# Optimization experiments

Hardware: AMD Instinct MI355X
Metric: run time of the kernel (lower is better)

Reference implementation:

```python
import jax, jax.numpy as jnp
import numpy as np

N_NODES = 20000
IN_DIM = 256
HID = 128
N_CLASSES = 64
N_EDGES = 320000
EPS_BN = 1e-5


def setup_inputs() -> dict:
    key = jax.random.key(0)
    ks = jax.random.split(key, 24)
    s = 0.1
    inp = {}
    inp['x'] = jax.random.normal(ks[0], (N_NODES, IN_DIM), dtype=jnp.float32)
    inp['edge_index'] = jax.random.randint(ks[1], (2, N_EDGES), 0, N_NODES, dtype=jnp.int32)
    # GATConv 1: in=IN_DIM, out=HID per head, heads=4, concat=False
    inp['W1'] = s * jax.random.normal(ks[2], (IN_DIM, 4 * HID), dtype=jnp.float32)
    inp['a_src1'] = s * jax.random.normal(ks[3], (4, HID), dtype=jnp.float32)
    inp['a_dst1'] = s * jax.random.normal(ks[4], (4, HID), dtype=jnp.float32)
    inp['b1'] = jnp.zeros((HID,), jnp.float32)
    # GATConv 2: in=HID, out=HID per head, heads=4, concat=False
    inp['W2'] = s * jax.random.normal(ks[5], (HID, 4 * HID), dtype=jnp.float32)
    inp['a_src2'] = s * jax.random.normal(ks[6], (4, HID), dtype=jnp.float32)
    inp['a_dst2'] = s * jax.random.normal(ks[7], (4, HID), dtype=jnp.float32)
    inp['b2'] = jnp.zeros((HID,), jnp.float32)
    # GATConv 3: heads=1, concat=True (default)
    inp['W3'] = s * jax.random.normal(ks[8], (HID, HID), dtype=jnp.float32)
    inp['a_src3'] = s * jax.random.normal(ks[9], (1, HID), dtype=jnp.float32)
    inp['a_dst3'] = s * jax.random.normal(ks[10], (1, HID), dtype=jnp.float32)
    inp['b3'] = jnp.zeros((HID,), jnp.float32)
    # BatchNorm (eval-mode running stats)
    for i, k in zip((1, 2), (ks[11], ks[12])):
        inp[f'bn{i}_g'] = jnp.ones((HID,), jnp.float32)
        inp[f'bn{i}_b'] = jnp.zeros((HID,), jnp.float32)
        inp[f'bn{i}_m'] = 0.01 * jax.random.normal(k, (HID,), dtype=jnp.float32)
        inp[f'bn{i}_v'] = jnp.ones((HID,), jnp.float32)
    # classifier MLP
    inp['l1_w'] = s * jax.random.normal(ks[13], (HID, HID), dtype=jnp.float32)
    inp['l1_b'] = jnp.zeros((HID,), jnp.float32)
    inp['l2_w'] = s * jax.random.normal(ks[14], (HID, HID // 2), dtype=jnp.float32)
    inp['l2_b'] = jnp.zeros((HID // 2,), jnp.float32)
    inp['l3_w'] = s * jax.random.normal(ks[15], (HID // 2, N_CLASSES), dtype=jnp.float32)
    inp['l3_b'] = jnp.zeros((N_CLASSES,), jnp.float32)
    return inp


def _gat(x, src, dst, W, a_src, a_dst, b, heads, out_ch, concat):
    """PyG GATConv (with self-loops already appended to src/dst)."""
    n = x.shape[0]
    h = (x @ W).reshape(n, heads, out_ch)            # [N,H,C]
    alpha_s = jnp.sum(h * a_src[None], axis=-1)       # [N,H]
    alpha_d = jnp.sum(h * a_dst[None], axis=-1)       # [N,H]
    e = jax.nn.leaky_relu(alpha_s[src] + alpha_d[dst], 0.2)  # [E,H]
    # segment softmax over incoming edges of each destination node
    m = jax.ops.segment_max(e, dst, num_segments=n)
    m = jnp.where(jnp.isfinite(m), m, 0.0)
    ex = jnp.exp(e - m[dst])
    den = jax.ops.segment_sum(ex, dst, num_segments=n)
    alpha = ex / (den[dst] + 1e-16)                   # [E,H]
    msg = h[src] * alpha[:, :, None]                  # [E,H,C]
    out = jax.ops.segment_sum(msg, dst, num_segments=n)  # [N,H,C]
    out = out.reshape(n, heads * out_ch) if concat else out.mean(axis=1)
    return out + b


def _bn_eval(x, g, b, m, v):
    return g * (x - m) * jax.lax.rsqrt(v + EPS_BN) + b


def reference(x, edge_index, W1, a_src1, a_dst1, b1, W2, a_src2, a_dst2, b2,
              W3, a_src3, a_dst3, b3, bn1_g, bn1_b, bn1_m, bn1_v,
              bn2_g, bn2_b, bn2_m, bn2_v, l1_w, l1_b, l2_w, l2_b, l3_w, l3_b):
    n = x.shape[0]
    loops = jnp.arange(n, dtype=edge_index.dtype)
    src = jnp.concatenate([edge_index[0], loops])
    dst = jnp.concatenate([edge_index[1], loops])

    h = _gat(x, src, dst, W1, a_src1, a_dst1, b1, 4, HID, False)
    h = jax.nn.relu(_bn_eval(h, bn1_g, bn1_b, bn1_m, bn1_v))
    h = _gat(h, src, dst, W2, a_src2, a_dst2, b2, 4, HID, False)
    h = jax.nn.relu(_bn_eval(h, bn2_g, bn2_b, bn2_m, bn2_v))
    h = _gat(h, src, dst, W3, a_src3, a_dst3, b3, 1, HID, True)

    h = jax.nn.relu(h @ l1_w + l1_b)
    h = jax.nn.relu(h @ l2_w + l2_b)
    return jax.nn.sigmoid(h @ l3_w + l3_b)  # [N, num_labels]
```

## Files before the change

### kernel.cpp

```cpp
#include <hip/hip_runtime.h>
#include <cstdint>
#include <cstddef>

#define NN 20000
#define CAP 96

typedef __bf16 bf16_t;
typedef __bf16 bf16x8 __attribute__((ext_vector_type(8)));
typedef float f32x4 __attribute__((ext_vector_type(4)));

#define AS1 __attribute__((address_space(1)))
#define AS3 __attribute__((address_space(3)))

__device__ __forceinline__ float lrelu(float x) { return x >= 0.f ? x : 0.2f * x; }
__device__ __forceinline__ float bflo(uint32_t u) { return __uint_as_float(u << 16); }
__device__ __forceinline__ float bfhi(uint32_t u) { return __uint_as_float(u & 0xffff0000u); }

__device__ __forceinline__ uint32_t pack2bf(float a, float b) {
  bf16_t x = (bf16_t)a, y = (bf16_t)b;
  uint16_t ux = __builtin_bit_cast(uint16_t, x);
  uint16_t uy = __builtin_bit_cast(uint16_t, y);
  return (uint32_t)ux | ((uint32_t)uy << 16);
}


struct WDesc { const float* W; bf16_t* Bt; int K; int Cw; int H; float scale; int b0; };
struct WPack { WDesc d[4]; };

struct Prep1Args {
  WPack wp;
  const float *W1, *as1, *ad1, *W2, *as2, *ad2, *W3, *as3, *ad3;
  float *P1, *P2, *P3;
  const float *W3m, *L1w, *b3v, *l1b;
  bf16_t* M3t; float* bm;
  const int* ei; int E, N, EB;
  int* cnt; int* col;
};

__global__ __launch_bounds__(256) void prep1(Prep1Args a) {
  __shared__ float tile[32][33];
  const int b = blockIdx.x;
  const int t = threadIdx.x;

  if (b < 204) {
    int i = 3;
#pragma unroll
    for (int k = 2; k >= 0; --k)
      if (b < a.wp.d[k + 1].b0) i = k;
    const WDesc de = a.wp.d[i];
    const int bi = b - de.b0;
    const int ktiles = de.K / 32;
    const int kt = bi % ktiles, rt = bi / ktiles;
    const int gc = rt * 32;
    const int h = gc / de.Cw, c0 = gc % de.Cw;
    const int tx = t & 31, ty = t >> 5;
#pragma unroll
    for (int r = 0; r < 32; r += 8)
      tile[ty + r][tx] = de.W[(size_t)(kt * 32 + ty + r) * (de.H * de.Cw) + h * de.Cw + c0 + tx];
    __syncthreads();
#pragma unroll
    for (int r = 0; r < 32; r += 8)
      de.Bt[(size_t)(c0 + ty + r) * (de.H * de.K) + h * de.K + kt * 32 + tx] =
          (bf16_t)(de.scale * tile[tx][ty + r]);
  } else if (b < 716) {
    const int kk = b - 204;
    const float *W, *asrc, *adst;
    float* P;
    int K, H, k;
    if (kk < 256)      { W = a.W1; asrc = a.as1; adst = a.ad1; P = a.P1; K = 256; H = 4; k = kk; }
    else if (kk < 384) { W = a.W2; asrc = a.as2; adst = a.ad2; P = a.P2; K = 128; H = 4; k = kk - 256; }
    else               { W = a.W3; asrc = a.as3; adst = a.ad3; P = a.P3; K = 128; H = 1; k = kk - 384; }
    for (int j = 0; j < 2 * H; ++j) {
      const int h = (j < H) ? j : j - H;
      const float* av = (j < H) ? asrc : adst;
      float pv = 0.f;
      if (t < 128) pv = W[(size_t)k * (H * 128) + h * 128 + t] * av[h * 128 + t];
#pragma unroll
      for (int d = 1; d < 64; d <<= 1) pv += __shfl_xor(pv, d);
      if (t == 0 || t == 64) tile[0][t >> 6] = pv;
      __syncthreads();
      if (t == 0) P[j * K + k] = tile[0][0] + tile[0][1];
      __syncthreads();
    }
  } else if (b < 780) {
    const int idx = (b - 716) * 256 + t;
    const int k = idx >> 7, c = idx & 127;
    float s = 0.f;
    for (int m = 0; m < 128; ++m) s += a.W3m[k * 128 + m] * a.L1w[m * 128 + c];
    a.M3t[c * 128 + k] = (bf16_t)s;
    if (k == 0) {
      float tt = a.l1b[c];
      for (int m = 0; m < 128; ++m) tt += a.b3v[m] * a.L1w[m * 128 + c];
      a.bm[c] = tt;
    }
  } else {
    const int i = (b - 780) * 256 + t;
    if (i < a.E + a.N) {
      int src, dst;
      if (i < a.E) { src = a.ei[i]; dst = a.ei[a.E + i]; }
      else         { src = i - a.E; dst = src; }
      int slot = atomicAdd(&a.cnt[dst], 1);
      a.col[(size_t)dst * CAP + slot] = src;
    }
  }
}


__global__ __launch_bounds__(256) void cast_alpha(const float* __restrict__ x,
                                                  const float* __restrict__ P1,
                                                  bf16_t* __restrict__ xb,
                                                  float* __restrict__ asadA) {
  const int b = blockIdx.x, t = threadIdx.x;
  const int wv = t >> 6, lane = t & 63;
  const int n = b * 4 + wv;
  const float4 v = *(const float4*)&x[(size_t)n * 256 + lane * 4];
  uint2 ov;
  ov.x = pack2bf(v.x, v.y);
  ov.y = pack2bf(v.z, v.w);
  *(uint2*)&xb[(size_t)n * 256 + lane * 4] = ov;
  float s[8];
#pragma unroll
  for (int j = 0; j < 8; ++j) {
    const float4 pj = *(const float4*)&P1[j * 256 + lane * 4];
    s[j] = v.x * pj.x + v.y * pj.y + v.z * pj.z + v.w * pj.w;
  }
#pragma unroll
  for (int j = 0; j < 8; ++j)
#pragma unroll
    for (int d = 1; d < 64; d <<= 1) s[j] += __shfl_xor(s[j], d);
  if (lane == 0) {
#pragma unroll
    for (int j = 0; j < 8; ++j) asadA[(size_t)n * 8 + j] = s[j];
  }
}


template <int ACT, int J, typename OUT_T>
__global__ __launch_bounds__(256) void gemm_mfma(const bf16_t* __restrict__ A,
                                                 const bf16_t* __restrict__ Bt,
                                                 const float* __restrict__ bias,
                                                 const float* __restrict__ bng,
                                                 const float* __restrict__ bnb,
                                                 const float* __restrict__ bnm,
                                                 const float* __restrict__ bnv,
                                                 OUT_T* __restrict__ C,
                                                 const float* __restrict__ Pa,
                                                 float* __restrict__ asad,
                                                 int M, int N, int K) {
  constexpr int TM = 32, TN = 128, BK = 64;
  constexpr int NRA = (TM * BK * 2) / 4096;
  constexpr int NRB = (TN * BK * 2) / 4096;
  __shared__ __align__(16) bf16_t As[TM * BK];
  __shared__ __align__(16) bf16_t Bs[TN * BK];

  const int t = threadIdx.x;
  const int wave = t >> 6, lane = t & 63;
  const int ln15 = lane & 15, quad = lane >> 4;
  const int bm = blockIdx.x * TM;
  const int wm = (wave >> 1) * 16;
  const int wn = (wave & 1) * 64;
  const int rowLimA = M - 1 - bm;
  const size_t strideAB = (size_t)K * 2;

  f32x4 acc[4];
#pragma unroll
  for (int ni = 0; ni < 4; ++ni) acc[ni] = (f32x4){0.f, 0.f, 0.f, 0.f};

  const char* gA = (const char*)(A + (size_t)bm * K);
  const char* gB = (const char*)Bt;

  for (int k0 = 0; k0 < K; k0 += BK) {
#pragma unroll
    for (int r = 0; r < NRA; ++r) {
      int base = (wave * NRA + r) * 1024;
      int flat = base + lane * 16;
      int row = flat >> 7;
      int grow = row < rowLimA ? row : rowLimA;
      const char* gp = gA + (size_t)grow * strideAB + (size_t)(k0 * 2) + (flat & 127);
      __builtin_amdgcn_global_load_lds((const AS1 void*)gp,
                                       (AS3 void*)((char*)As + base), 16, 0, 0);
    }
#pragma unroll
    for (int r = 0; r < NRB; ++r) {
      int base = (wave * NRB + r) * 1024;
      int flat = base + lane * 16;
      int row = flat >> 7;
      const char* gp = gB + (size_t)row * strideAB + (size_t)(k0 * 2) + (flat & 127);
      __builtin_amdgcn_global_load_lds((const AS1 void*)gp,
                                       (AS3 void*)((char*)Bs + base), 16, 0, 0);
    }
    __syncthreads();
#pragma unroll
    for (int kk = 0; kk < BK; kk += 32) {
      bf16x8 af, bfr[4];
      af = *(const bf16x8*)&As[(wm + ln15) * BK + kk + quad * 8];
#pragma unroll
      for (int ni = 0; ni < 4; ++ni)
        bfr[ni] = *(const bf16x8*)&Bs[(wn + ni * 16 + ln15) * BK + kk + quad * 8];
#pragma unroll
      for (int ni = 0; ni < 4; ++ni)
        acc[ni] = __builtin_amdgcn_mfma_f32_16x16x32_bf16(af, bfr[ni], acc[ni], 0, 0, 0);
    }
    __syncthreads();
  }

  {
    int r0 = bm + wm + quad * 4;
#pragma unroll
    for (int ni = 0; ni < 4; ++ni) {
      int c = wn + ni * 16 + ln15;
      float bv = bias ? bias[c] : 0.f;
      float sc = 1.f, sh = 0.f;
      if (ACT == 3) {
        sc = bng[c] * rsqrtf(bnv[c] + 1e-5f);
        sh = bnb[c] - bnm[c] * sc;
      }
#pragma unroll
      for (int reg = 0; reg < 4; ++reg) {
        int r = r0 + reg;
        float v = acc[ni][reg] + bv;
        if (ACT == 1) v = fmaxf(v, 0.f);
        else if (ACT == 3) v = fmaxf(v * sc + sh, 0.f);
        acc[ni][reg] = v;
        if (r < M) C[(size_t)r * N + c] = (OUT_T)v;
      }
    }
  }

  if (J > 0) {
#pragma unroll
    for (int j = 0; j < J; ++j) {
      float pj[4];
#pragma unroll
      for (int ni = 0; ni < 4; ++ni)
        pj[ni] = Pa[j * 128 + wn + ni * 16 + ln15];
      float s[4];
#pragma unroll
      for (int reg = 0; reg < 4; ++reg)
        s[reg] = acc[0][reg] * pj[0] + acc[1][reg] * pj[1] +
                 acc[2][reg] * pj[2] + acc[3][reg] * pj[3];
#pragma unroll
      for (int d = 1; d < 16; d <<= 1)
#pragma unroll
        for (int reg = 0; reg < 4; ++reg)
          s[reg] += __shfl_xor(s[reg], d);
      if (ln15 == 0) {
#pragma unroll
        for (int reg = 0; reg < 4; ++reg) {
          int r = bm + wm + quad * 4 + reg;
          if (r < M) atomicAdd(&asad[(size_t)r * J + j], s[reg]);
        }
      }
    }
  }
}


template <int K>
__global__ __launch_bounds__(128) void gat_agg_in4(const bf16_t* __restrict__ f,
                                                   const float* __restrict__ asad,
                                                   const int* __restrict__ cnt,
                                                   const int* __restrict__ col,
                                                   bf16_t* __restrict__ agg) {
  constexpr int KC = K / 64;
  const int wv = threadIdx.x >> 6, lane = threadIdx.x & 63;
  const int n = blockIdx.x * 2 + wv;
  __shared__ int sb[2][64];
  __shared__ float4 wl[2][64];

  const int r0 = n * CAP;
  const int deg = cnt[n];
  const int r1 = r0 + deg;
  const float4 adv = *(const float4*)&asad[(size_t)n * 8 + 4];
  const char* fb = (const char*)f;
  const size_t loff = (size_t)lane * (KC * 2);

  float acc[4][KC];
#pragma unroll
  for (int j = 0; j < 4; ++j)
#pragma unroll
    for (int q = 0; q < KC; ++q) acc[j][q] = 0.f;

  auto edge_fma = [&](const char* gp, float4 w4) {
    if (KC == 4) {
      uint2 b = *(const uint2*)gp;
      float v0 = bflo(b.x), v1 = bfhi(b.x), v2 = bflo(b.y), v3 = bfhi(b.y);
      acc[0][0] += w4.x * v0; acc[0][1] += w4.x * v1; acc[0][2] += w4.x * v2; acc[0][3] += w4.x * v3;
      acc[1][0] += w4.y * v0; acc[1][1] += w4.y * v1; acc[1][2] += w4.y * v2; acc[1][3] += w4.y * v3;
      acc[2][0] += w4.z * v0; acc[2][1] += w4.z * v1; acc[2][2] += w4.z * v2; acc[2][3] += w4.z * v3;
      acc[3][0] += w4.w * v0; acc[3][1] += w4.w * v1; acc[3][2] += w4.w * v2; acc[3][3] += w4.w * v3;
    } else {
      uint32_t b = *(const uint32_t*)gp;
      float v0 = bflo(b), v1 = bfhi(b);
      acc[0][0] += w4.x * v0; acc[0][1] += w4.x * v1;
      acc[1][0] += w4.y * v0; acc[1][1] += w4.y * v1;
      acc[2][0] += w4.z * v0; acc[2][1] += w4.z * v1;
      acc[3][0] += w4.w * v0; acc[3][1] += w4.w * v1;
    }
  };

  if (deg <= 64) {
    const bool valid = lane < deg;
    int s = n;
    float e0 = -1e30f, e1 = -1e30f, e2 = -1e30f, e3 = -1e30f;
    if (valid) {
      s = col[r0 + lane];
      const float4 av = *(const float4*)&asad[(size_t)s * 8];
      e0 = lrelu(av.x + adv.x); e1 = lrelu(av.y + adv.y);
      e2 = lrelu(av.z + adv.z); e3 = lrelu(av.w + adv.w);
    }
    float m0 = e0, m1 = e1, m2 = e2, m3 = e3;
#pragma unroll
    for (int d = 1; d < 64; d <<= 1) {
      m0 = fmaxf(m0, __shfl_xor(m0, d)); m1 = fmaxf(m1, __shfl_xor(m1, d));
      m2 = fmaxf(m2, __shfl_xor(m2, d)); m3 = fmaxf(m3, __shfl_xor(m3, d));
    }
    float x0 = valid ? __expf(e0 - m0) : 0.f;
    float x1 = valid ? __expf(e1 - m1) : 0.f;
    float x2 = valid ? __expf(e2 - m2) : 0.f;
    float x3 = valid ? __expf(e3 - m3) : 0.f;
    float d0 = x0, d1 = x1, d2 = x2, d3 = x3;
#pragma unroll
    for (int d = 1; d < 64; d <<= 1) {
      d0 += __shfl_xor(d0, d); d1 += __shfl_xor(d1, d);
      d2 += __shfl_xor(d2, d); d3 += __shfl_xor(d3, d);
    }
    sb[wv][lane] = s * (K * 2);
    wl[wv][lane] = valid ? make_float4(x0 / (d0 + 1e-16f), x1 / (d1 + 1e-16f),
                                       x2 / (d2 + 1e-16f), x3 / (d3 + 1e-16f))
                         : make_float4(0.f, 0.f, 0.f, 0.f);
    __builtin_amdgcn_wave_barrier();

    const int nb = (deg + 7) >> 3;
    uint2 bA[8], bB[8];
    auto loadb = [&](int g, uint2* b) {
#pragma unroll
      for (int k = 0; k < 8; ++k) {
        const char* gp = fb + (size_t)sb[wv][g + k] + loff;
        if (KC == 4) b[k] = *(const uint2*)gp;
        else         b[k].x = *(const uint32_t*)gp;
      }
    };
    auto fmab = [&](int g, const uint2* b) {
#pragma unroll
      for (int k = 0; k < 8; ++k) {
        const float4 w = wl[wv][g + k];
        if (KC == 4) {
          float v0 = bflo(b[k].x), v1 = bfhi(b[k].x), v2 = bflo(b[k].y), v3 = bfhi(b[k].y);
          acc[0][0] += w.x * v0; acc[0][1] += w.x * v1; acc[0][2] += w.x * v2; acc[0][3] += w.x * v3;
          acc[1][0] += w.y * v0; acc[1][1] += w.y * v1; acc[1][2] += w.y * v2; acc[1][3] += w.y * v3;
          acc[2][0] += w.z * v0; acc[2][1] += w.z * v1; acc[2][2] += w.z * v2; acc[2][3] += w.z * v3;
          acc[3][0] += w.w * v0; acc[3][1] += w.w * v1; acc[3][2] += w.w * v2; acc[3][3] += w.w * v3;
        } else {
          float v0 = bflo(b[k].x), v1 = bfhi(b[k].x);
          acc[0][0] += w.x * v0; acc[0][1] += w.x * v1;
          acc[1][0] += w.y * v0; acc[1][1] += w.y * v1;
          acc[2][0] += w.z * v0; acc[2][1] += w.z * v1;
          acc[3][0] += w.w * v0; acc[3][1] += w.w * v1;
        }
      }
    };
    loadb(0, bA);
    int i = 0;
    while (i + 2 <= nb) {
      loadb((i + 1) * 8, bB);
      fmab(i * 8, bA);
      if (i + 2 < nb) loadb((i + 2) * 8, bA);
      fmab((i + 1) * 8, bB);
      i += 2;
    }
    if (i < nb) fmab(i * 8, bA);
  } else {
    float m0 = -1e30f, m1 = -1e30f, m2 = -1e30f, m3 = -1e30f;
    for (int i = r0 + lane; i < r1; i += 64) {
      const float4 av = *(const float4*)&asad[(size_t)col[i] * 8];
      m0 = fmaxf(m0, lrelu(av.x + adv.x)); m1 = fmaxf(m1, lrelu(av.y + adv.y));
      m2 = fmaxf(m2, lrelu(av.z + adv.z)); m3 = fmaxf(m3, lrelu(av.w + adv.w));
    }
#pragma unroll
    for (int d = 1; d < 64; d <<= 1) {
      m0 = fmaxf(m0, __shfl_xor(m0, d)); m1 = fmaxf(m1, __shfl_xor(m1, d));
      m2 = fmaxf(m2, __shfl_xor(m2, d)); m3 = fmaxf(m3, __shfl_xor(m3, d));
    }
    float d0 = 0.f, d1 = 0.f, d2 = 0.f, d3 = 0.f;
    for (int i = r0 + lane; i < r1; i += 64) {
      const float4 av = *(const float4*)&asad[(size_t)col[i] * 8];
      d0 += __expf(lrelu(av.x + adv.x) - m0); d1 += __expf(lrelu(av.y + adv.y) - m1);
      d2 += __expf(lrelu(av.z + adv.z) - m2); d3 += __expf(lrelu(av.w + adv.w) - m3);
    }
#pragma unroll
    for (int d = 1; d < 64; d <<= 1) {
      d0 += __shfl_xor(d0, d); d1 += __shfl_xor(d1, d);
      d2 += __shfl_xor(d2, d); d3 += __shfl_xor(d3, d);
    }
    const float i0 = 1.f / (d0 + 1e-16f), i1 = 1.f / (d1 + 1e-16f);
    const float i2 = 1.f / (d2 + 1e-16f), i3 = 1.f / (d3 + 1e-16f);
    for (int base = r0; base < r1; base += 64) {
      const int ne = min(64, r1 - base);
      if (lane < ne) {
        const int s = col[base + lane];
        const float4 av = *(const float4*)&asad[(size_t)s * 8];
        sb[wv][lane] = s * (K * 2);
        wl[wv][lane] = make_float4(__expf(lrelu(av.x + adv.x) - m0) * i0,
                                   __expf(lrelu(av.y + adv.y) - m1) * i1,
                                   __expf(lrelu(av.z + adv.z) - m2) * i2,
                                   __expf(lrelu(av.w + adv.w) - m3) * i3);
      }
      __builtin_amdgcn_wave_barrier();
      for (int g = 0; g < ne; ++g)
        edge_fma(fb + (size_t)sb[wv][g] + loff, wl[wv][g]);
      __builtin_amdgcn_wave_barrier();
    }
  }

#pragma unroll
  for (int j = 0; j < 4; ++j) {
    if (KC == 4) {
      uint2 ov;
      ov.x = pack2bf(acc[j][0], acc[j][1]);
      ov.y = pack2bf(acc[j][2], acc[j][3]);
      *(uint2*)&agg[(size_t)n * (4 * K) + j * K + lane * 4] = ov;
    } else {
      *(uint32_t*)&agg[(size_t)n * (4 * K) + j * K + lane * 2] = pack2bf(acc[j][0], acc[j][1]);
    }
  }
}


__global__ __launch_bounds__(128) void gat_agg_in1(const bf16_t* __restrict__ f,
                                                   const float* __restrict__ asad,
                                                   const int* __restrict__ cnt,
                                                   const int* __restrict__ col,
                                                   bf16_t* __restrict__ agg) {
  const int wv = threadIdx.x >> 6, lane = threadIdx.x & 63;
  const int n = blockIdx.x * 2 + wv;
  __shared__ int sb[2][64];
  __shared__ float wl[2][64];

  const int r0 = n * CAP;
  const int deg = cnt[n];
  const int r1 = r0 + deg;
  const float adv = asad[(size_t)n * 2 + 1];
  const char* fb = (const char*)f;
  const size_t loff = (size_t)lane * 4;
  float a0 = 0.f, a1 = 0.f;

  auto fma2 = [&](uint32_t v, float w) { a0 += w * bflo(v); a1 += w * bfhi(v); };

  if (deg <= 64) {
    const bool valid = lane < deg;
    int s = n;
    float e = -1e30f;
    if (valid) { s = col[r0 + lane]; e = lrelu(asad[(size_t)s * 2] + adv); }
    float m = e;
#pragma unroll
    for (int d = 1; d < 64; d <<= 1) m = fmaxf(m, __shfl_xor(m, d));
    float x = valid ? __expf(e - m) : 0.f;
    float den = x;
#pragma unroll
    for (int d = 1; d < 64; d <<= 1) den += __shfl_xor(den, d);
    sb[wv][lane] = s * 256;
    wl[wv][lane] = valid ? x / (den + 1e-16f) : 0.f;
    __builtin_amdgcn_wave_barrier();

    const int nb = (deg + 7) >> 3;
    uint32_t bA[8], bB[8];
    auto loadb = [&](int g, uint32_t* b) {
#pragma unroll
      for (int k = 0; k < 8; ++k)
        b[k] = *(const uint32_t*)(fb + (size_t)sb[wv][g + k] + loff);
    };
    auto fmab = [&](int g, const uint32_t* b) {
#pragma unroll
      for (int k = 0; k < 8; ++k) {
        const float w = wl[wv][g + k];
        a0 += w * bflo(b[k]); a1 += w * bfhi(b[k]);
      }
    };
    loadb(0, bA);
    int i = 0;
    while (i + 2 <= nb) {
      loadb((i + 1) * 8, bB);
      fmab(i * 8, bA);
      if (i + 2 < nb) loadb((i + 2) * 8, bA);
      fmab((i + 1) * 8, bB);
      i += 2;
    }
    if (i < nb) fmab(i * 8, bA);
  } else {
    float m = -1e30f;
    for (int i = r0 + lane; i < r1; i += 64) m = fmaxf(m, lrelu(asad[(size_t)col[i] * 2] + adv));
#pragma unroll
    for (int d = 1; d < 64; d <<= 1) m = fmaxf(m, __shfl_xor(m, d));
    float den = 0.f;
    for (int i = r0 + lane; i < r1; i += 64) den += __expf(lrelu(asad[(size_t)col[i] * 2] + adv) - m);
#pragma unroll
    for (int d = 1; d < 64; d <<= 1) den += __shfl_xor(den, d);
    const float dinv = 1.f / (den + 1e-16f);
    for (int base = r0; base < r1; base += 64) {
      const int ne = min(64, r1 - base);
      if (lane < ne) {
        const int s = col[base + lane];
        sb[wv][lane] = s * 256;
        wl[wv][lane] = __expf(lrelu(asad[(size_t)s * 2] + adv) - m) * dinv;
      }
      __builtin_amdgcn_wave_barrier();
      for (int g = 0; g < ne; ++g)
        fma2(*(const uint32_t*)(fb + (size_t)sb[wv][g] + loff), wl[wv][g]);
      __builtin_amdgcn_wave_barrier();
    }
  }
  *(uint32_t*)&agg[(size_t)n * 128 + lane * 2] = pack2bf(a0, a1);
}


__global__ __launch_bounds__(256) void mlp_tail(const bf16_t* __restrict__ A,
                                                const bf16_t* __restrict__ M3t,
                                                const float* __restrict__ bm,
                                                const bf16_t* __restrict__ l2t,
                                                const float* __restrict__ l2b,
                                                const bf16_t* __restrict__ l3t,
                                                const float* __restrict__ l3b,
                                                float* __restrict__ out, int M) {
  __shared__ __align__(16) bf16_t As[128 * 128];
  __shared__ __align__(16) bf16_t Ws[128 * 128];
  const int t = threadIdx.x, wave = t >> 6, lane = t & 63;
  const int ln15 = lane & 15, quad = lane >> 4;
  const int bmr = blockIdx.x * 128;
  const int rowLim = M - 1 - bmr;

#pragma unroll
  for (int r = 0; r < 8; ++r) {
    int base = (wave * 8 + r) * 1024;
    int flat = base + lane * 16;
    int row = flat >> 8;
    int grow = row < rowLim ? row : rowLim;
    const char* gp = (const char*)A + (size_t)grow * 256 + (flat & 255);
    __builtin_amdgcn_global_load_lds((const AS1 void*)gp,
                                     (AS3 void*)((char*)As + base), 16, 0, 0);
  }
#pragma unroll
  for (int r = 0; r < 8; ++r) {
    int base = (wave * 8 + r) * 1024;
    __builtin_amdgcn_global_load_lds((const AS1 void*)((const char*)M3t + base + lane * 16),
                                     (AS3 void*)((char*)Ws + base), 16, 0, 0);
  }
  __syncthreads();

  const int wm = wave * 32;
  f32x4 a1[2][8];
#pragma unroll
  for (int mi = 0; mi < 2; ++mi)
#pragma unroll
    for (int ni = 0; ni < 8; ++ni) a1[mi][ni] = (f32x4){0.f, 0.f, 0.f, 0.f};
#pragma unroll
  for (int kk = 0; kk < 128; kk += 32) {
    bf16x8 af[2];
#pragma unroll
    for (int mi = 0; mi < 2; ++mi)
      af[mi] = *(const bf16x8*)&As[(wm + mi * 16 + ln15) * 128 + kk + quad * 8];
#pragma unroll
    for (int ni = 0; ni < 8; ++ni) {
      bf16x8 bf = *(const bf16x8*)&Ws[(ni * 16 + ln15) * 128 + kk + quad * 8];
#pragma unroll
      for (int mi = 0; mi < 2; ++mi)
        a1[mi][ni] = __builtin_amdgcn_mfma_f32_16x16x32_bf16(af[mi], bf, a1[mi][ni], 0, 0, 0);
    }
  }
  __syncthreads();

#pragma unroll
  for (int r = 0; r < 4; ++r) {
    int base = (wave * 4 + r) * 1024;
    __builtin_amdgcn_global_load_lds((const AS1 void*)((const char*)l2t + base + lane * 16),
                                     (AS3 void*)((char*)Ws + base), 16, 0, 0);
  }
#pragma unroll
  for (int r = 0; r < 2; ++r) {
    int base = (wave * 2 + r) * 1024;
    __builtin_amdgcn_global_load_lds((const AS1 void*)((const char*)l3t + base + lane * 16),
                                     (AS3 void*)((char*)Ws + 8192 * 2 + base), 16, 0, 0);
  }
#pragma unroll
  for (int mi = 0; mi < 2; ++mi) {
    int r0 = wm + mi * 16 + quad * 4;
#pragma unroll
    for (int ni = 0; ni < 8; ++ni) {
      int c = ni * 16 + ln15;
      float bv = bm[c];
#pragma unroll
      for (int reg = 0; reg < 4; ++reg)
        As[(r0 + reg) * 128 + c] = (bf16_t)fmaxf(a1[mi][ni][reg] + bv, 0.f);
    }
  }
  __syncthreads();

  f32x4 a2[2][4];
#pragma unroll
  for (int mi = 0; mi < 2; ++mi)
#pragma unroll
    for (int ni = 0; ni < 4; ++ni) a2[mi][ni] = (f32x4){0.f, 0.f, 0.f, 0.f};
#pragma unroll
  for (int kk = 0; kk < 128; kk += 32) {
    bf16x8 af[2];
#pragma unroll
    for (int mi = 0; mi < 2; ++mi)
      af[mi] = *(const bf16x8*)&As[(wm + mi * 16 + ln15) * 128 + kk + quad * 8];
#pragma unroll
    for (int ni = 0; ni < 4; ++ni) {
      bf16x8 bf = *(const bf16x8*)&Ws[(ni * 16 + ln15) * 128 + kk + quad * 8];
#pragma unroll
      for (int mi = 0; mi < 2; ++mi)
        a2[mi][ni] = __builtin_amdgcn_mfma_f32_16x16x32_bf16(af[mi], bf, a2[mi][ni], 0, 0, 0);
    }
  }
  __syncthreads();

#pragma unroll
  for (int mi = 0; mi < 2; ++mi) {
    int r0 = wm + mi * 16 + quad * 4;
#pragma unroll
    for (int ni = 0; ni < 4; ++ni) {
      int c = ni * 16 + ln15;
      float bv = l2b[c];
#pragma unroll
      for (int reg = 0; reg < 4; ++reg)
        As[(r0 + reg) * 64 + c] = (bf16_t)fmaxf(a2[mi][ni][reg] + bv, 0.f);
    }
  }
  __syncthreads();

  f32x4 a3[2][4];
#pragma unroll
  for (int mi = 0; mi < 2; ++mi)
#pragma unroll
    for (int ni = 0; ni < 4; ++ni) a3[mi][ni] = (f32x4){0.f, 0.f, 0.f, 0.f};
#pragma unroll
  for (int kk = 0; kk < 64; kk += 32) {
    bf16x8 af[2];
#pragma unroll
    for (int mi = 0; mi < 2; ++mi)
      af[mi] = *(const bf16x8*)&As[(wm + mi * 16 + ln15) * 64 + kk + quad * 8];
#pragma unroll
    for (int ni = 0; ni < 4; ++ni) {
      bf16x8 bf = *(const bf16x8*)&Ws[8192 + (ni * 16 + ln15) * 64 + kk + quad * 8];
#pragma unroll
      for (int mi = 0; mi < 2; ++mi)
        a3[mi][ni] = __builtin_amdgcn_mfma_f32_16x16x32_bf16(af[mi], bf, a3[mi][ni], 0, 0, 0);
    }
  }
#pragma unroll
  for (int mi = 0; mi < 2; ++mi) {
    int r0 = wm + mi * 16 + quad * 4;
#pragma unroll
    for (int ni = 0; ni < 4; ++ni) {
      int c = ni * 16 + ln15;
      float bv = l3b[c];
#pragma unroll
      for (int reg = 0; reg < 4; ++reg) {
        int r = bmr + r0 + reg;
        if (r < M) {
          float v = a3[mi][ni][reg] + bv;
          out[(size_t)r * 64 + c] = 1.f / (1.f + __expf(-v));
        }
      }
    }
  }
}


extern "C" void kernel_launch(void* const* d_in, const int* in_sizes, int n_in,
                              void* d_out, int out_size, void* d_ws, size_t ws_size,
                              hipStream_t stream) {
  const float* x      = (const float*)d_in[0];
  const int*   ei     = (const int*)d_in[1];
  const float* W1     = (const float*)d_in[2];
  const float* a_src1 = (const float*)d_in[3];
  const float* a_dst1 = (const float*)d_in[4];
  const float* b1     = (const float*)d_in[5];
  const float* W2     = (const float*)d_in[6];
  const float* a_src2 = (const float*)d_in[7];
  const float* a_dst2 = (const float*)d_in[8];
  const float* b2     = (const float*)d_in[9];
  const float* W3     = (const float*)d_in[10];
  const float* a_src3 = (const float*)d_in[11];
  const float* a_dst3 = (const float*)d_in[12];
  const float* b3     = (const float*)d_in[13];
  const float* bn1g = (const float*)d_in[14];
  const float* bn1b = (const float*)d_in[15];
  const float* bn1m = (const float*)d_in[16];
  const float* bn1v = (const float*)d_in[17];
  const float* bn2g = (const float*)d_in[18];
  const float* bn2b = (const float*)d_in[19];
  const float* bn2m = (const float*)d_in[20];
  const float* bn2v = (const float*)d_in[21];
  const float* l1w = (const float*)d_in[22];
  const float* l1b = (const float*)d_in[23];
  const float* l2w = (const float*)d_in[24];
  const float* l2b = (const float*)d_in[25];
  const float* l3w = (const float*)d_in[26];
  const float* l3b = (const float*)d_in[27];
  float* out = (float*)d_out;

  const int N = NN;
  const int E = in_sizes[1] / 2;
  const int ET = E + N;
  const int EB = (ET + 255) / 256;

  char* p = (char*)d_ws;
  auto carve = [&](size_t bytes) {
    char* q = p;
    p += (bytes + 255) & ~(size_t)255;
    return q;
  };
  bf16_t* xb    = (bf16_t*)carve((size_t)N * 256 * 2);
  bf16_t* aggb  = (bf16_t*)carve((size_t)N * 1024 * 2);
  bf16_t* f1b   = (bf16_t*)carve((size_t)N * 128 * 2);
  bf16_t* f2b   = (bf16_t*)carve((size_t)N * 128 * 2);
  float* asadA  = (float*)carve((size_t)N * 8 * 4);
  int* cnt      = (int*)carve((size_t)N * 4);
  float* asadB  = (float*)carve((size_t)N * 8 * 4);
  float* asadC  = (float*)carve((size_t)N * 2 * 4);
  const size_t zbytes = (size_t)(p - (char*)cnt);
  int* col      = (int*)carve((size_t)N * CAP * 4);
  bf16_t* Ws1t  = (bf16_t*)carve((size_t)128 * 1024 * 2);
  bf16_t* Ws2t  = (bf16_t*)carve((size_t)128 * 512 * 2);
  bf16_t* M3t   = (bf16_t*)carve((size_t)128 * 128 * 2);
  bf16_t* l2t   = (bf16_t*)carve((size_t)64 * 128 * 2);
  bf16_t* l3t   = (bf16_t*)carve((size_t)64 * 64 * 2);
  float* P1     = (float*)carve((size_t)8 * 256 * 4);
  float* P2     = (float*)carve((size_t)8 * 128 * 4);
  float* P3     = (float*)carve((size_t)2 * 128 * 4);
  float* bm     = (float*)carve((size_t)128 * 4);
  (void)ws_size; (void)n_in; (void)out_size;

  hipMemsetAsync(cnt, 0, zbytes, stream);

  Prep1Args pa;
  pa.wp.d[0] = {W1,  Ws1t, 256, 128, 4, 0.25f, 0};
  pa.wp.d[1] = {W2,  Ws2t, 128, 128, 4, 0.25f, 128};
  pa.wp.d[2] = {l2w, l2t,  128, 64,  1, 1.0f,  192};
  pa.wp.d[3] = {l3w, l3t,  64,  64,  1, 1.0f,  200};
  pa.W1 = W1; pa.as1 = a_src1; pa.ad1 = a_dst1;
  pa.W2 = W2; pa.as2 = a_src2; pa.ad2 = a_dst2;
  pa.W3 = W3; pa.as3 = a_src3; pa.ad3 = a_dst3;
  pa.P1 = P1; pa.P2 = P2; pa.P3 = P3;
  pa.W3m = W3; pa.L1w = l1w; pa.b3v = b3; pa.l1b = l1b;
  pa.M3t = M3t; pa.bm = bm;
  pa.ei = ei; pa.E = E; pa.N = N; pa.EB = EB;
  pa.cnt = cnt; pa.col = col;
  prep1<<<780 + EB, 256, 0, stream>>>(pa);

  cast_alpha<<<N / 4, 256, 0, stream>>>(x, P1, xb, asadA);

  const int gm32 = (N + 31) / 32;
  const int gm   = (N + 127) / 128;
  const int gb   = N / 2;

  gat_agg_in4<256><<<gb, 128, 0, stream>>>(xb, asadA, cnt, col, aggb);
  gemm_mfma<3, 8, bf16_t><<<dim3(gm32, 1), 256, 0, stream>>>(
      aggb, Ws1t, b1, bn1g, bn1b, bn1m, bn1v, f1b, P2, asadB, N, 128, 1024);

  gat_agg_in4<128><<<gb, 128, 0, stream>>>(f1b, asadB, cnt, col, aggb);
  gemm_mfma<3, 2, bf16_t><<<dim3(gm32, 1), 256, 0, stream>>>(
      aggb, Ws2t, b2, bn2g, bn2b, bn2m, bn2v, f2b, P3, asadC, N, 128, 512);

  gat_agg_in1<<<gb, 128, 0, stream>>>(f2b, asadC, cnt, col, aggb);
  mlp_tail<<<gm, 256, 0, stream>>>(aggb, M3t, bm, l2t, l2b, l3t, l3b, out, N);
}
```

Baseline: 284.3 us.

## Fuse layer-2 GAT aggregation into the following MFMA GEMM kernel

Replaces the separate layer-2 aggregation kernel and its GEMM with one kernel. Each block first aggregates 32 nodes (softmax attention over neighbours, 4 heads) into a swizzled LDS tile, then runs the bf16 MFMA GEMM with the BN+ReLU epilogue and the attention-projection atomics. This removes the global write and re-read of the intermediate aggregated tensor and one kernel launch. The cost is much less parallelism in the gather phase: 625 blocks of 256 threads, each wave handling 8 nodes serially, against the previous 10000-block aggregation launch.

```diff
diff --git a/kernel.cpp b/kernel.cpp
--- a/kernel.cpp
+++ b/kernel.cpp
@@ -228,6 +228,252 @@
   }
 
   if (J > 0) {
+#pragma unroll
+    for (int j = 0; j < J; ++j) {
+      float pj[4];
+#pragma unroll
+      for (int ni = 0; ni < 4; ++ni)
+        pj[ni] = Pa[j * 128 + wn + ni * 16 + ln15];
+      float s[4];
+#pragma unroll
+      for (int reg = 0; reg < 4; ++reg)
+        s[reg] = acc[0][reg] * pj[0] + acc[1][reg] * pj[1] +
+                 acc[2][reg] * pj[2] + acc[3][reg] * pj[3];
+#pragma unroll
+      for (int d = 1; d < 16; d <<= 1)
+#pragma unroll
+        for (int reg = 0; reg < 4; ++reg)
+          s[reg] += __shfl_xor(s[reg], d);
+      if (ln15 == 0) {
+#pragma unroll
+        for (int reg = 0; reg < 4; ++reg) {
+          int r = bm + wm + quad * 4 + reg;
+          if (r < M) atomicAdd(&asad[(size_t)r * J + j], s[reg]);
+        }
+      }
+    }
+  }
+}
+
+
+__global__ __launch_bounds__(256) void fused_l2(const bf16_t* __restrict__ f,
+                                                const float* __restrict__ asadB,
+                                                const int* __restrict__ cnt,
+                                                const int* __restrict__ col,
+                                                const bf16_t* __restrict__ Bt,
+                                                const float* __restrict__ bias,
+                                                const float* __restrict__ bng,
+                                                const float* __restrict__ bnb,
+                                                const float* __restrict__ bnm,
+                                                const float* __restrict__ bnv,
+                                                bf16_t* __restrict__ C,
+                                                const float* __restrict__ Pa,
+                                                float* __restrict__ asad,
+                                                int M, int N, int K) {
+  __shared__ __align__(16) bf16_t Af[32 * 512];
+  __shared__ __align__(16) bf16_t Bs[128 * 64];
+  __shared__ int sb[4][64];
+  __shared__ float4 wl[4][64];
+
+  const int t = threadIdx.x;
+  const int wave = t >> 6, lane = t & 63;
+  const int ln15 = lane & 15, quad = lane >> 4;
+  const char* fb = (const char*)f;
+  const size_t loff = (size_t)lane * 4;
+
+  for (int i = 0; i < 8; ++i) {
+    const int n = blockIdx.x * 32 + wave * 8 + i;
+    const int lrow = wave * 8 + i;
+    const int r0 = n * CAP;
+    const int deg = cnt[n];
+    const int r1 = r0 + deg;
+    const float4 adv = *(const float4*)&asadB[(size_t)n * 8 + 4];
+
+    float acc[4][2];
+#pragma unroll
+    for (int j = 0; j < 4; ++j) { acc[j][0] = 0.f; acc[j][1] = 0.f; }
+
+    if (deg <= 64) {
+      const bool valid = lane < deg;
+      int s = n;
+      float e0 = -1e30f, e1 = -1e30f, e2 = -1e30f, e3 = -1e30f;
+      if (valid) {
+        s = col[r0 + lane];
+        const float4 av = *(const float4*)&asadB[(size_t)s * 8];
+        e0 = lrelu(av.x + adv.x); e1 = lrelu(av.y + adv.y);
+        e2 = lrelu(av.z + adv.z); e3 = lrelu(av.w + adv.w);
+      }
+      float m0 = e0, m1 = e1, m2 = e2, m3 = e3;
+#pragma unroll
+      for (int d = 1; d < 64; d <<= 1) {
+        m0 = fmaxf(m0, __shfl_xor(m0, d)); m1 = fmaxf(m1, __shfl_xor(m1, d));
+        m2 = fmaxf(m2, __shfl_xor(m2, d)); m3 = fmaxf(m3, __shfl_xor(m3, d));
+      }
+      float x0 = valid ? __expf(e0 - m0) : 0.f;
+      float x1 = valid ? __expf(e1 - m1) : 0.f;
+      float x2 = valid ? __expf(e2 - m2) : 0.f;
+      float x3 = valid ? __expf(e3 - m3) : 0.f;
+      float d0 = x0, d1 = x1, d2 = x2, d3 = x3;
+#pragma unroll
+      for (int d = 1; d < 64; d <<= 1) {
+        d0 += __shfl_xor(d0, d); d1 += __shfl_xor(d1, d);
+        d2 += __shfl_xor(d2, d); d3 += __shfl_xor(d3, d);
+      }
+      sb[wave][lane] = s * 256;
+      wl[wave][lane] = valid ? make_float4(x0 / (d0 + 1e-16f), x1 / (d1 + 1e-16f),
+                                           x2 / (d2 + 1e-16f), x3 / (d3 + 1e-16f))
+                             : make_float4(0.f, 0.f, 0.f, 0.f);
+      __builtin_amdgcn_wave_barrier();
+
+      const int nb = (deg + 7) >> 3;
+      uint32_t bA[8], bB[8];
+      auto loadb = [&](int g, uint32_t* b) {
+#pragma unroll
+        for (int k = 0; k < 8; ++k)
+          b[k] = *(const uint32_t*)(fb + (size_t)sb[wave][g + k] + loff);
+      };
+      auto fmab = [&](int g, const uint32_t* b) {
+#pragma unroll
+        for (int k = 0; k < 8; ++k) {
+          const float4 w = wl[wave][g + k];
+          float v0 = bflo(b[k]), v1 = bfhi(b[k]);
+          acc[0][0] += w.x * v0; acc[0][1] += w.x * v1;
+          acc[1][0] += w.y * v0; acc[1][1] += w.y * v1;
+          acc[2][0] += w.z * v0; acc[2][1] += w.z * v1;
+          acc[3][0] += w.w * v0; acc[3][1] += w.w * v1;
+        }
+      };
+      loadb(0, bA);
+      int ii = 0;
+      while (ii + 2 <= nb) {
+        loadb((ii + 1) * 8, bB);
+        fmab(ii * 8, bA);
+        if (ii + 2 < nb) loadb((ii + 2) * 8, bA);
+        fmab((ii + 1) * 8, bB);
+        ii += 2;
+      }
+      if (ii < nb) fmab(ii * 8, bA);
+      __builtin_amdgcn_wave_barrier();
+    } else {
+      float m0 = -1e30f, m1 = -1e30f, m2 = -1e30f, m3 = -1e30f;
+      for (int q = r0 + lane; q < r1; q += 64) {
+        const float4 av = *(const float4*)&asadB[(size_t)col[q] * 8];
+        m0 = fmaxf(m0, lrelu(av.x + adv.x)); m1 = fmaxf(m1, lrelu(av.y + adv.y));
+        m2 = fmaxf(m2, lrelu(av.z + adv.z)); m3 = fmaxf(m3, lrelu(av.w + adv.w));
+      }
+#pragma unroll
+      for (int d = 1; d < 64; d <<= 1) {
+        m0 = fmaxf(m0, __shfl_xor(m0, d)); m1 = fmaxf(m1, __shfl_xor(m1, d));
+        m2 = fmaxf(m2, __shfl_xor(m2, d)); m3 = fmaxf(m3, __shfl_xor(m3, d));
+      }
+      float d0 = 0.f, d1 = 0.f, d2 = 0.f, d3 = 0.f;
+      for (int q = r0 + lane; q < r1; q += 64) {
+        const float4 av = *(const float4*)&asadB[(size_t)col[q] * 8];
+        d0 += __expf(lrelu(av.x + adv.x) - m0); d1 += __expf(lrelu(av.y + adv.y) - m1);
+        d2 += __expf(lrelu(av.z + adv.z) - m2); d3 += __expf(lrelu(av.w + adv.w) - m3);
+      }
+#pragma unroll
+      for (int d = 1; d < 64; d <<= 1) {
+        d0 += __shfl_xor(d0, d); d1 += __shfl_xor(d1, d);
+        d2 += __shfl_xor(d2, d); d3 += __shfl_xor(d3, d);
+      }
+      const float i0 = 1.f / (d0 + 1e-16f), i1 = 1.f / (d1 + 1e-16f);
+      const float i2 = 1.f / (d2 + 1e-16f), i3 = 1.f / (d3 + 1e-16f);
+      for (int base = r0; base < r1; base += 64) {
+        const int ne = min(64, r1 - base);
+        if (lane < ne) {
+          const int s = col[base + lane];
+          const float4 av = *(const float4*)&asadB[(size_t)s * 8];
+          sb[wave][lane] = s * 256;
+          wl[wave][lane] = make_float4(__expf(lrelu(av.x + adv.x) - m0) * i0,
+                                       __expf(lrelu(av.y + adv.y) - m1) * i1,
+                                       __expf(lrelu(av.z + adv.z) - m2) * i2,
+                                       __expf(lrelu(av.w + adv.w) - m3) * i3);
+        }
+        __builtin_amdgcn_wave_barrier();
+        for (int g = 0; g < ne; ++g) {
+          uint32_t b = *(const uint32_t*)(fb + (size_t)sb[wave][g] + loff);
+          const float4 w = wl[wave][g];
+          float v0 = bflo(b), v1 = bfhi(b);
+          acc[0][0] += w.x * v0; acc[0][1] += w.x * v1;
+          acc[1][0] += w.y * v0; acc[1][1] += w.y * v1;
+          acc[2][0] += w.z * v0; acc[2][1] += w.z * v1;
+          acc[3][0] += w.w * v0; acc[3][1] += w.w * v1;
+        }
+        __builtin_amdgcn_wave_barrier();
+      }
+    }
+
+    const unsigned xr = (unsigned)((lrow & 7) << 4);
+#pragma unroll
+    for (int j = 0; j < 4; ++j) {
+      unsigned off = (unsigned)(lrow * 1024 + j * 256 + lane * 4) ^ xr;
+      *(uint32_t*)((char*)Af + off) = pack2bf(acc[j][0], acc[j][1]);
+    }
+  }
+  __syncthreads();
+
+  constexpr int TN = 128, BK = 64;
+  constexpr int NRB = (TN * BK * 2) / 4096;
+  const int bm = blockIdx.x * 32;
+  const int wm = (wave >> 1) * 16;
+  const int wn = (wave & 1) * 64;
+  const size_t strideB = (size_t)K * 2;
+  const char* gB = (const char*)Bt;
+
+  f32x4 acc[4];
+#pragma unroll
+  for (int ni = 0; ni < 4; ++ni) acc[ni] = (f32x4){0.f, 0.f, 0.f, 0.f};
+
+  for (int k0 = 0; k0 < K; k0 += BK) {
+#pragma unroll
+    for (int r = 0; r < NRB; ++r) {
+      int base = (wave * NRB + r) * 1024;
+      int flat = base + lane * 16;
+      int row = flat >> 7;
+      const char* gp = gB + (size_t)row * strideB + (size_t)(k0 * 2) + (flat & 127);
+      __builtin_amdgcn_global_load_lds((const AS1 void*)gp,
+                                       (AS3 void*)((char*)Bs + base), 16, 0, 0);
+    }
+    __syncthreads();
+#pragma unroll
+    for (int kk = 0; kk < BK; kk += 32) {
+      const int arow = wm + ln15;
+      unsigned abyte = (unsigned)(arow * 1024 + (k0 + kk) * 2 + quad * 16) ^
+                       (unsigned)((arow & 7) << 4);
+      bf16x8 af = *(const bf16x8*)((const char*)Af + abyte);
+      bf16x8 bfr[4];
+#pragma unroll
+      for (int ni = 0; ni < 4; ++ni)
+        bfr[ni] = *(const bf16x8*)&Bs[(wn + ni * 16 + ln15) * BK + kk + quad * 8];
+#pragma unroll
+      for (int ni = 0; ni < 4; ++ni)
+        acc[ni] = __builtin_amdgcn_mfma_f32_16x16x32_bf16(af, bfr[ni], acc[ni], 0, 0, 0);
+    }
+    __syncthreads();
+  }
+
+  {
+    int r0 = bm + wm + quad * 4;
+#pragma unroll
+    for (int ni = 0; ni < 4; ++ni) {
+      int c = wn + ni * 16 + ln15;
+      float bv = bias ? bias[c] : 0.f;
+      float sc = bng[c] * rsqrtf(bnv[c] + 1e-5f);
+      float sh = bnb[c] - bnm[c] * sc;
+#pragma unroll
+      for (int reg = 0; reg < 4; ++reg) {
+        int r = r0 + reg;
+        float v = acc[ni][reg] + bv;
+        v = fmaxf(v * sc + sh, 0.f);
+        acc[ni][reg] = v;
+        if (r < M) C[(size_t)r * N + c] = (bf16_t)v;
+      }
+    }
+  }
+
+  {
+    constexpr int J = 2;
 #pragma unroll
     for (int j = 0; j < J; ++j) {
       float pj[4];
@@ -761,9 +1007,9 @@
   gemm_mfma<3, 8, bf16_t><<<dim3(gm32, 1), 256, 0, stream>>>(
       aggb, Ws1t, b1, bn1g, bn1b, bn1m, bn1v, f1b, P2, asadB, N, 128, 1024);
 
-  gat_agg_in4<128><<<gb, 128, 0, stream>>>(f1b, asadB, cnt, col, aggb);
-  gemm_mfma<3, 2, bf16_t><<<dim3(gm32, 1), 256, 0, stream>>>(
-      aggb, Ws2t, b2, bn2g, bn2b, bn2m, bn2v, f2b, P3, asadC, N, 128, 512);
+  fused_l2<<<gm32, 256, 0, stream>>>(f1b, asadB, cnt, col, Ws2t, b2,
+                                     bn2g, bn2b, bn2m, bn2v, f2b, P3, asadC,
+                                     N, 128, 512);
 
   gat_agg_in1<<<gb, 128, 0, stream>>>(f2b, asadC, cnt, col, aggb);
   mlp_tail<<<gm, 256, 0, stream>>>(aggb, M3t, bm, l2t, l2b, l3t, l3b, out, N);
```

Result: slower. 310.8 us (+9.3%).
